# Kernel tuning notes

Hardware: AMD Instinct MI355X
Metric: run time of the kernel (lower is better)

## Reference

```python
import jax, jax.numpy as jnp
import numpy as np

EMB = 1280
MD = 200
N = 20000
E = 200000
LN_EPS = 1e-5


def _layer_norm(x, g, b):
    mu = jnp.mean(x, axis=-1, keepdims=True)
    var = jnp.mean((x - mu) ** 2, axis=-1, keepdims=True)
    return (x - mu) * jax.lax.rsqrt(var + LN_EPS) * g + b


def _gat_conv(x, edge_index, edge_attr, W, We, a_src, a_dst, a_edge, bias, heads, C):
    """PyG GATConv (bias-free lin, edge_dim, add_self_loops with fill='mean')."""
    n = x.shape[0]
    src, dst = edge_index[0], edge_index[1]
    # self-loop edge_attr = mean of incoming edge_attr per dst node (0 if none)
    cnt = jax.ops.segment_sum(jnp.ones((edge_attr.shape[0],), x.dtype), dst, n)
    s = jax.ops.segment_sum(edge_attr, dst, n)
    loop_attr = jnp.where(cnt[:, None] > 0, s / jnp.maximum(cnt, 1.0)[:, None], 0.0)
    loop = jnp.arange(n)
    src = jnp.concatenate([src, loop])
    dst = jnp.concatenate([dst, loop])
    ea = jnp.concatenate([edge_attr, loop_attr], axis=0)
    h = (x @ W).reshape(n, heads, C)                      # [N,H,C]
    al_s = jnp.einsum('nhc,hc->nh', h, a_src)
    al_d = jnp.einsum('nhc,hc->nh', h, a_dst)
    eh = (ea @ We).reshape(-1, heads, C)                  # [E+N,H,C]
    al_e = jnp.einsum('ehc,hc->eh', eh, a_edge)
    alpha = jax.nn.leaky_relu(al_s[src] + al_d[dst] + al_e, 0.2)
    amax = jax.ops.segment_max(alpha, dst, n)
    amax = jnp.where(jnp.isfinite(amax), amax, 0.0)
    ex = jnp.exp(alpha - amax[dst])
    denom = jax.ops.segment_sum(ex, dst, n)
    w = ex / (denom[dst] + 1e-16)                         # segment softmax over dst
    out = jax.ops.segment_sum(h[src] * w[:, :, None], dst, n)
    return out.reshape(n, heads * C) + bias


def _forward(x, edge_index, edge_attr,
             ca_qw, ca_qb, ca_kw, ca_kb, ca_vw, ca_vb, ca_ow, ca_ob,
             g0_w, g0_ew, g0_as, g0_ad, g0_ae, g0_b, ln0_g, ln0_b,
             g1_w, g1_ew, g1_as, g1_ad, g1_ae, g1_b, ln1_g, ln1_b,
             g2_w, g2_ew, g2_as, g2_ad, g2_ae, g2_b, ln2_g, ln2_b,
             cls_w1, cls_b1, cls_w2, cls_b2):
    xe = x[:, :EMB]
    md = x[0, EMB:]
    # CrossAttention: single md vector -> K,V are [1,hidden]
    Q = xe @ ca_qw + ca_qb                                # [N,hid]
    K = md @ ca_kw + ca_kb                                # [hid]
    V = md @ ca_vw + ca_vb                                # [hid]
    scores = (Q @ K) / jnp.sqrt(jnp.asarray(Q.shape[-1], Q.dtype))  # [N]
    wts = jax.nn.softmax(scores, axis=0)[:, None]         # softmax over nodes
    attended = wts * V[None, :]                           # [N,hid]
    h = attended @ ca_ow + ca_ob + xe                     # [N,EMB]

    h = _gat_conv(h, edge_index, edge_attr, g0_w, g0_ew, g0_as, g0_ad, g0_ae, g0_b, 4, 256)
    h = jax.nn.relu(_layer_norm(h, ln0_g, ln0_b))
    h = _gat_conv(h, edge_index, edge_attr, g1_w, g1_ew, g1_as, g1_ad, g1_ae, g1_b, 4, 256)
    h = jax.nn.relu(_layer_norm(h, ln1_g, ln1_b))
    h = _gat_conv(h, edge_index, edge_attr, g2_w, g2_ew, g2_as, g2_ad, g2_ae, g2_b, 1, 256)
    h = jax.nn.relu(_layer_norm(h, ln2_g, ln2_b))

    g = jnp.mean(h, axis=0, keepdims=True)                # [1,256]
    g = jax.nn.relu(g @ cls_w1 + cls_b1)
    return g @ cls_w2 + cls_b2                            # [1,2]


def setup_inputs() -> dict:
    key = jax.random.key(0)
    ks = jax.random.split(key, 64)
    i = [0]
    def nrm(shape, scale=0.05):
        i[0] += 1
        return jax.random.normal(ks[i[0]], shape, jnp.float32) * scale
    inp = {}
    inp['x'] = nrm((N, EMB + MD), 1.0)
    inp['edge_index'] = jax.random.randint(ks[60], (2, E), 0, N, jnp.int64 if jax.config.read('jax_enable_x64') else jnp.int32)
    inp['edge_attr'] = jax.random.uniform(ks[61], (E, 1), jnp.float32)
    inp.update(ca_qw=nrm((EMB, 256)), ca_qb=jnp.zeros((256,), jnp.float32),
               ca_kw=nrm((MD, 256)), ca_kb=jnp.zeros((256,), jnp.float32),
               ca_vw=nrm((MD, 256)), ca_vb=jnp.zeros((256,), jnp.float32),
               ca_ow=nrm((256, EMB)), ca_ob=jnp.zeros((EMB,), jnp.float32))
    inp.update(g0_w=nrm((EMB, 1024)), g0_ew=nrm((1, 1024)), g0_as=nrm((4, 256)),
               g0_ad=nrm((4, 256)), g0_ae=nrm((4, 256)), g0_b=jnp.zeros((1024,), jnp.float32),
               ln0_g=jnp.ones((1024,), jnp.float32), ln0_b=jnp.zeros((1024,), jnp.float32))
    inp.update(g1_w=nrm((1024, 1024)), g1_ew=nrm((1, 1024)), g1_as=nrm((4, 256)),
               g1_ad=nrm((4, 256)), g1_ae=nrm((4, 256)), g1_b=jnp.zeros((1024,), jnp.float32),
               ln1_g=jnp.ones((1024,), jnp.float32), ln1_b=jnp.zeros((1024,), jnp.float32))
    inp.update(g2_w=nrm((1024, 256)), g2_ew=nrm((1, 256)), g2_as=nrm((1, 256)),
               g2_ad=nrm((1, 256)), g2_ae=nrm((1, 256)), g2_b=jnp.zeros((256,), jnp.float32),
               ln2_g=jnp.ones((256,), jnp.float32), ln2_b=jnp.zeros((256,), jnp.float32))
    inp.update(cls_w1=nrm((256, 128)), cls_b1=jnp.zeros((128,), jnp.float32),
               cls_w2=nrm((128, 2)), cls_b2=jnp.zeros((2,), jnp.float32))
    return inp


def reference(x, edge_index, edge_attr,
              ca_qw, ca_qb, ca_kw, ca_kb, ca_vw, ca_vb, ca_ow, ca_ob,
              g0_w, g0_ew, g0_as, g0_ad, g0_ae, g0_b, ln0_g, ln0_b,
              g1_w, g1_ew, g1_as, g1_ad, g1_ae, g1_b, ln1_g, ln1_b,
              g2_w, g2_ew, g2_as, g2_ad, g2_ae, g2_b, ln2_g, ln2_b,
              cls_w1, cls_b1, cls_w2, cls_b2):
    return _forward(x, edge_index, edge_attr,
                    ca_qw, ca_qb, ca_kw, ca_kb, ca_vw, ca_vb, ca_ow, ca_ob,
                    g0_w, g0_ew, g0_as, g0_ad, g0_ae, g0_b, ln0_g, ln0_b,
                    g1_w, g1_ew, g1_as, g1_ad, g1_ae, g1_b, ln1_g, ln1_b,
                    g2_w, g2_ew, g2_as, g2_ad, g2_ae, g2_b, ln2_g, ln2_b,
                    cls_w1, cls_b1, cls_w2, cls_b2)
```

## Files before the change

### kernel.cpp

```cpp
#include <hip/hip_runtime.h>
#include <hip/hip_bf16.h>
#include <math.h>

#define N_NODES 20000
#define N_EDGES 200000
#define XROW    1480

typedef __attribute__((ext_vector_type(8))) _Float16 f16x8;
typedef __attribute__((ext_vector_type(8))) unsigned short u16x8;
typedef __attribute__((ext_vector_type(4))) float f32x4v;

__device__ __forceinline__ float wsum(float v){
#pragma unroll
  for (int o=32;o>0;o>>=1) v += __shfl_down(v,o);
  return v;
}
__device__ __forceinline__ float wmax(float v){
#pragma unroll
  for (int o=32;o>0;o>>=1) v = fmaxf(v,__shfl_down(v,o));
  return v;
}
__device__ __forceinline__ float wsum_all(float v){
#pragma unroll
  for (int o=32;o>0;o>>=1) v += __shfl_xor(v,o);
  return v;
}
__device__ __forceinline__ float wmax_all(float v){
#pragma unroll
  for (int o=32;o>0;o>>=1) v = fmaxf(v,__shfl_xor(v,o));
  return v;
}

__device__ __forceinline__ unsigned short f2hu(float f){
  _Float16 h = (_Float16)f;
  return __builtin_bit_cast(unsigned short, h);
}
__device__ __forceinline__ float hu2f(unsigned short u){
  return (float)__builtin_bit_cast(_Float16, u);
}

__device__ __forceinline__ void async_copy16(void* lds, const void* g){
  __builtin_amdgcn_global_load_lds((const __attribute__((address_space(1))) void*)g,
                                   (__attribute__((address_space(3))) void*)lds, 16, 0, 0);
}

__global__ void edge_count_kernel(const int* __restrict__ ei, const float* __restrict__ ea,
                                  int* __restrict__ cnt, float* __restrict__ easum, int E){
  int e = blockIdx.x*256 + threadIdx.x;
  if (e >= E) return;
  int dst = ei[E + e];
  atomicAdd(&cnt[dst], 1);
  atomicAdd(&easum[dst], ea[e]);
}

__launch_bounds__(1024)
__global__ void scan_kernel(const int* __restrict__ cnt, const float* __restrict__ easum,
                            int* __restrict__ off, float* __restrict__ loop_attr, int n){
  __shared__ int buf[1024];
  const int PER = (N_NODES + 1023)/1024;
  int t = threadIdx.x;
  int base = t*PER;
  int local[PER];
  int s = 0;
#pragma unroll
  for (int k=0;k<PER;k++){
    int i = base + k;
    int v = (i<n)? cnt[i] : 0;
    local[k] = v;
    s += v;
  }
  buf[t] = s;
  __syncthreads();
  for (int d2=1; d2<1024; d2<<=1){
    int tv = (t>=d2)? buf[t-d2] : 0;
    __syncthreads();
    buf[t] += tv;
    __syncthreads();
  }
  int run = buf[t] - s;
#pragma unroll
  for (int k=0;k<PER;k++){
    int i = base + k;
    if (i < n){
      off[i] = run;
      int v = local[k];
      loop_attr[i] = (v>0) ? easum[i]/(float)v : 0.f;
      run += v;
    }
  }
  if (t == 1023) off[n] = buf[1023];
}

__global__ void edge_fill_kernel(const int* __restrict__ ei, const float* __restrict__ ea,
                                 const int* __restrict__ off, int* __restrict__ fill,
                                 int* __restrict__ csr_src, float* __restrict__ csr_ea, int E){
  int e = blockIdx.x*256 + threadIdx.x;
  if (e >= E) return;
  int dst = ei[E + e];
  int pos = off[dst] + atomicAdd(&fill[dst], 1);
  csr_src[pos] = ei[e];
  csr_ea[pos]  = ea[e];
}

__global__ void wt_f16_kernel(const float* __restrict__ W, int K, int N,
                              unsigned short* __restrict__ Wt){
  __shared__ float tile[32][33];
  int k0 = blockIdx.x*32, n0 = blockIdx.y*32;
  int tx = threadIdx.x & 31, ty = threadIdx.x >> 5;
  for (int r=ty; r<32; r+=8) tile[r][tx] = W[(size_t)(k0+r)*N + n0+tx];
  __syncthreads();
  for (int r=ty; r<32; r+=8){
    float w = tile[tx][r];
    Wt[(size_t)(n0+r)*K + k0+tx] = f2hu(w);
  }
}

__global__ void kv_kernel(const float* __restrict__ x,
                          const float* __restrict__ kw, const float* __restrict__ kb,
                          const float* __restrict__ vw, const float* __restrict__ vb,
                          float* __restrict__ Kv, float* __restrict__ Vv){
  int j = threadIdx.x;
  float ka = kb[j], va = vb[j];
  for (int k=0;k<200;k++){
    float m = x[1280+k];
    ka = fmaf(m, kw[k*256+j], ka);
    va = fmaf(m, vw[k*256+j], va);
  }
  Kv[j]=ka; Vv[j]=va;
}

__global__ void qkvo_kernel(const float* __restrict__ qw, const float* __restrict__ ow,
                            const float* __restrict__ Kv, const float* __restrict__ Vv,
                            float* __restrict__ qK, float* __restrict__ Vo){
  int idx = blockIdx.x*256 + threadIdx.x;
  if (idx < 1280){
    float a=0;
    for (int j=0;j<256;j++) a = fmaf(qw[idx*256+j], Kv[j], a);
    qK[idx]=a;
  } else if (idx < 2560){
    int j = idx-1280;
    float a=0;
    for (int i=0;i<256;i++) a = fmaf(Vv[i], ow[(size_t)i*1280+j], a);
    Vo[j]=a;
  }
}

__global__ void obw_kernel(const float* __restrict__ ob, const float* __restrict__ Vo,
                           const float* __restrict__ W, float* __restrict__ obW, float* __restrict__ VoW){
  int j = blockIdx.x*256 + threadIdx.x;
  float a=0,b=0;
  for (int i=0;i<1280;i++){
    float w = W[(size_t)i*1024+j];
    a = fmaf(ob[i], w, a);
    b = fmaf(Vo[i], w, b);
  }
  obW[j]=a; VoW[j]=b;
}

__launch_bounds__(256)
__global__ void xh_scores_kernel(const float* __restrict__ x, const float* __restrict__ qK,
                                 unsigned short* __restrict__ xh, float* __restrict__ scores, int n){
  __shared__ float qs[1280];
  int t = threadIdx.x;
  for (int i=t;i<1280;i+=256) qs[i]=qK[i];
  __syncthreads();
  int wid = t>>6, lane = t&63;
  int node = blockIdx.x*4 + wid;
  if (node >= n) return;
  const float* xr = x + (size_t)node*XROW;
  unsigned short* orow = xh + (size_t)node*1280;
  float acc = 0.f;
#pragma unroll
  for (int it=0; it<5; it++){
    int c4 = it*64 + lane;
    float4 v = *(const float4*)(xr + c4*4);
    ushort4 o;
    o.x = f2hu(v.x); o.y = f2hu(v.y); o.z = f2hu(v.z); o.w = f2hu(v.w);
    *(ushort4*)(orow + c4*4) = o;
    acc = fmaf(v.x, qs[c4*4+0], acc);
    acc = fmaf(v.y, qs[c4*4+1], acc);
    acc = fmaf(v.z, qs[c4*4+2], acc);
    acc = fmaf(v.w, qs[c4*4+3], acc);
  }
  acc = wsum(acc);
  if (lane==0) scores[node] = acc;
}

__launch_bounds__(1024)
__global__ void softmax_nodes(const float* __restrict__ scores, float* __restrict__ wts, int n){
  __shared__ float red[16];
  int t = threadIdx.x, lane=t&63, wid=t>>6;
  float m = -INFINITY;
  for (int i=t;i<n;i+=1024) m = fmaxf(m, scores[i]);
  m = wmax(m);
  if (lane==0) red[wid]=m;
  __syncthreads();
  if (t==0){ float r=red[0]; for (int k=1;k<16;k++) r=fmaxf(r,red[k]); red[0]=r; }
  __syncthreads();
  float M = red[0];
  __syncthreads();
  float z=0;
  for (int i=t;i<n;i+=1024) z += __expf((scores[i]-M)*(1.f/16.f));
  z = wsum(z);
  if (lane==0) red[wid]=z;
  __syncthreads();
  if (t==0){ float r=0; for (int k=0;k<16;k++) r+=red[k]; red[0]=r; }
  __syncthreads();
  float invZ = 1.f/red[0];
  for (int i=t;i<n;i+=1024) wts[i] = __expf((scores[i]-M)*(1.f/16.f))*invZ;
}

__launch_bounds__(256)
__global__ void gemm_f16(const unsigned short* __restrict__ A,
                         const unsigned short* __restrict__ B,
                         unsigned short* __restrict__ C, int M, int N, int K,
                         const float* __restrict__ addCol,
                         const float* __restrict__ vCol,
                         const float* __restrict__ wRow,
                         const float* __restrict__ a_src,
                         const float* __restrict__ a_dst,
                         float* __restrict__ alsp,
                         float* __restrict__ aldp)
{
  __shared__ short lds[2*2*128*64];

  const int ntc = N >> 7;
  const int sh  = __popc(ntc - 1);
  const int g   = blockIdx.y >> sh;
  const int nt  = blockIdx.y & (ntc - 1);
  const int band = blockIdx.x + (g << 3);
  if (band * 128 >= M) return;

  const int t = threadIdx.x;
  const int w = t>>6, l = t&63;
  const int bm = band*128, bn = nt*128;
  const int wr = (w>>1)*64, wc = (w&1)*64;
  const int half = w & 1;

  f32x4v acc[4][4];
#pragma unroll
  for (int i=0;i<4;i++)
#pragma unroll
    for (int j=0;j<4;j++) acc[i][j] = (f32x4v){0.f,0.f,0.f,0.f};

  const unsigned short* Ap[4]; const unsigned short* Bp[4];
  int ldsOff[4];
#pragma unroll
  for (int q=0;q<4;q++){
    int p  = (w*4+q)*64 + l;
    int r  = p>>3, pc = p&7;
    int kc = (pc ^ (r&7))*8;
    int rowA = bm + r; if (rowA > M-1) rowA = M-1;
    Ap[q] = A + (size_t)rowA*K + kc;
    Bp[q] = B + (size_t)(bn+r)*K + kc;
    ldsOff[q] = (w*4+q)*64*8;
  }

  const int nsteps = K >> 6;

#pragma unroll
  for (int q=0;q<4;q++) async_copy16(lds + ldsOff[q],        Ap[q]);
#pragma unroll
  for (int q=0;q<4;q++) async_copy16(lds + 8192 + ldsOff[q], Bp[q]);

  const int q4 = l>>4, m16 = l&15;

  for (int ks0=0; ks0<nsteps; ++ks0){
    short* curb = lds + (ks0&1)*16384;

    if (ks0+1 < nsteps){
      short* nxt = lds + ((ks0+1)&1)*16384;
      const int k0n = (ks0+1)*64;
#pragma unroll
      for (int q=0;q<4;q++) async_copy16(nxt + ldsOff[q],        Ap[q] + k0n);
#pragma unroll
      for (int q=0;q<4;q++) async_copy16(nxt + 8192 + ldsOff[q], Bp[q] + k0n);
      asm volatile("s_waitcnt vmcnt(8)" ::: "memory");
    } else {
      asm volatile("s_waitcnt vmcnt(0)" ::: "memory");
    }
    __builtin_amdgcn_sched_barrier(0);
    __builtin_amdgcn_s_barrier();
    __builtin_amdgcn_sched_barrier(0);

    __builtin_amdgcn_s_setprio(1);
#pragma unroll
    for (int ks=0; ks<2; ks++){
      f16x8 af[4], bf[4];
      const int c = ks*4 + q4;
#pragma unroll
      for (int i=0;i<4;i++){
        int ra = wr + i*16 + m16;
        af[i] = *(const f16x8*)&curb[ra*64 + ((c ^ (ra&7))*8)];
        int rb = wc + i*16 + m16;
        bf[i] = *(const f16x8*)&curb[8192 + rb*64 + ((c ^ (rb&7))*8)];
      }
#pragma unroll
      for (int i=0;i<4;i++)
#pragma unroll
        for (int j=0;j<4;j++)
          acc[i][j] = __builtin_amdgcn_mfma_f32_16x16x32_f16(af[i], bf[j], acc[i][j], 0,0,0);
    }
    __builtin_amdgcn_s_setprio(0);
    __builtin_amdgcn_sched_barrier(0);
    __builtin_amdgcn_s_barrier();
    __builtin_amdgcn_sched_barrier(0);
  }

  float* sred = (float*)lds;
  float* dred = sred + 256;
  float asv[4], adv[4];
#pragma unroll
  for (int j=0;j<4;j++){
    int n = bn + wc + j*16 + m16;
    asv[j] = a_src[n];
    adv[j] = a_dst[n];
  }
#pragma unroll
  for (int i=0;i<4;i++){
#pragma unroll
    for (int r=0;r<4;r++){
      int rloc = wr + i*16 + q4*4 + r;
      int m = bm + rloc;
      float wrow = addCol ? wRow[m < M ? m : M-1] : 0.f;
      float vj[4];
#pragma unroll
      for (int j=0;j<4;j++){
        int n = bn + wc + j*16 + m16;
        float v = acc[i][j][r];
        if (addCol) v += addCol[n] + wrow*vCol[n];
        vj[j] = v;
      }
      if (m < M){
        unsigned short* crow = C + (size_t)m*N;
#pragma unroll
        for (int j=0;j<4;j++) crow[bn + wc + j*16 + m16] = f2hu(vj[j]);
      }
      float s = vj[0]*asv[0] + vj[1]*asv[1] + vj[2]*asv[2] + vj[3]*asv[3];
      float d = vj[0]*adv[0] + vj[1]*adv[1] + vj[2]*adv[2] + vj[3]*adv[3];
#pragma unroll
      for (int o=1;o<16;o<<=1){ s += __shfl_xor(s,o); d += __shfl_xor(d,o); }
      if (m16 == 0){
        sred[half*128 + rloc] = s;
        dred[half*128 + rloc] = d;
      }
    }
  }
  __syncthreads();
  if (t < 128){
    int m = bm + t;
    if (m < M){
      alsp[(size_t)nt*M + m] = sred[t] + sred[128+t];
      aldp[(size_t)nt*M + m] = dred[t] + dred[128+t];
    }
  }
}

__global__ void als_combine(const float* __restrict__ alsp, const float* __restrict__ aldp,
                            float* __restrict__ als, float* __restrict__ ald, int M, int H,
                            const float* __restrict__ We, const float* __restrict__ a_edge,
                            float* __restrict__ we){
  if (blockIdx.x == 0){
    int wid = threadIdx.x>>6, lane = threadIdx.x&63;
    if (wid < H){
      const float4* w4 = (const float4*)(We + wid*256);
      const float4* a4 = (const float4*)(a_edge + wid*256);
      float4 a = w4[lane], b = a4[lane];
      float v = a.x*b.x + a.y*b.y + a.z*b.z + a.w*b.w;
      v = wsum(v);
      if (lane==0) we[wid]=v;
    }
  }
  int idx = blockIdx.x*256 + threadIdx.x;
  if (idx >= M*H) return;
  int m = idx / H, hh = idx - m*H;
  als[idx] = alsp[(size_t)(2*hh)*M + m] + alsp[(size_t)(2*hh+1)*M + m];
  ald[idx] = aldp[(size_t)(2*hh)*M + m] + aldp[(size_t)(2*hh+1)*M + m];
}

template<int H>
__launch_bounds__(256)
__global__ void gat_agg_ln_wave(const unsigned short* __restrict__ hmat,
                           const float* __restrict__ als, const float* __restrict__ ald,
                           const int* __restrict__ off, const int* __restrict__ csr_src,
                           const float* __restrict__ csr_ea, const float* __restrict__ loop_attr,
                           const float* __restrict__ we,
                           const float* __restrict__ bias,
                           const float* __restrict__ ln_g, const float* __restrict__ ln_b,
                           float* __restrict__ outf, unsigned short* __restrict__ outb, int n)
{
  constexpr int OUT = 256*H;
  constexpr int CPL = OUT/64;
  const int wv = threadIdx.x>>6, lane = threadIdx.x&63;
  const int i = blockIdx.x*4 + wv;
  __shared__ float wbuf_s[4][64*H];
  __shared__ int   sbuf_s[4][64];
  if (i >= n) return;
  float* wbuf = wbuf_s[wv];
  int*   sbuf = sbuf_s[wv];

  const int begin = off[i];
  const int deg   = off[i+1]-begin;
  const int S     = deg + 1;

  float aldi[H], wei[H];
#pragma unroll
  for (int hh=0;hh<H;hh++){ aldi[hh]=ald[(size_t)i*H+hh]; wei[hh]=we[hh]; }
  const float lea = loop_attr[i];

  const int head = (lane*CPL) >> 8;
  const int c0   = lane*CPL;
  float acc[CPL];
#pragma unroll
  for (int c=0;c<CPL;c++) acc[c]=0.f;

  if (S <= 64){
    int src = i; float ev = lea;
    if (lane < deg){ src = csr_src[begin+lane]; ev = csr_ea[begin+lane]; }
    const bool act = lane < S;
    sbuf[lane] = src;

    if constexpr (CPL==16){
      u16x8 a0r0,a0r1,a1r0,a1r1;
      {
        const unsigned short* r0p = hmat + (size_t)sbuf[0]*OUT + c0;
        a0r0 = *(const u16x8*)r0p; a0r1 = *(const u16x8*)(r0p+8);
        a1r0 = a0r0; a1r1 = a0r1;
        if (S > 1){
          const unsigned short* r1p = hmat + (size_t)sbuf[1]*OUT + c0;
          a1r0 = *(const u16x8*)r1p; a1r1 = *(const u16x8*)(r1p+8);
        }
      }
      float a[H];
#pragma unroll
      for (int hh=0;hh<H;hh++){
        float v = als[(size_t)src*H+hh] + aldi[hh] + ev*wei[hh];
        a[hh] = v>0.f ? v : 0.2f*v;
      }
#pragma unroll
      for (int hh=0;hh<H;hh++){
        float M = wmax_all(act ? a[hh] : -INFINITY);
        float e = act ? __expf(a[hh]-M) : 0.f;
        float Z = wsum_all(e);
        wbuf[lane*H+hh] = e / (Z + 1e-16f);
      }
      int j = 0;
      for (; j+2<S; j+=2){
        u16x8 n0r0,n0r1,n1r0,n1r1;
        {
          const unsigned short* rp = hmat + (size_t)sbuf[j+2]*OUT + c0;
          n0r0 = *(const u16x8*)rp; n0r1 = *(const u16x8*)(rp+8);
          n1r0 = n0r0; n1r1 = n0r1;
          if (j+3 < S){
            const unsigned short* rq = hmat + (size_t)sbuf[j+3]*OUT + c0;
            n1r0 = *(const u16x8*)rq; n1r1 = *(const u16x8*)(rq+8);
          }
        }
        float w0 = wbuf[j*H+head], w1 = wbuf[(j+1)*H+head];
#pragma unroll
        for (int c=0;c<8;c++){
          acc[c]   = fmaf(w0, hu2f(a0r0[c]), acc[c]);
          acc[8+c] = fmaf(w0, hu2f(a0r1[c]), acc[8+c]);
        }
#pragma unroll
        for (int c=0;c<8;c++){
          acc[c]   = fmaf(w1, hu2f(a1r0[c]), acc[c]);
          acc[8+c] = fmaf(w1, hu2f(a1r1[c]), acc[8+c]);
        }
        a0r0=n0r0; a0r1=n0r1; a1r0=n1r0; a1r1=n1r1;
      }
      {
        float w0 = wbuf[j*H+head];
#pragma unroll
        for (int c=0;c<8;c++){
          acc[c]   = fmaf(w0, hu2f(a0r0[c]), acc[c]);
          acc[8+c] = fmaf(w0, hu2f(a0r1[c]), acc[8+c]);
        }
        if (j+1 < S){
          float w1 = wbuf[(j+1)*H+head];
#pragma unroll
          for (int c=0;c<8;c++){
            acc[c]   = fmaf(w1, hu2f(a1r0[c]), acc[c]);
            acc[8+c] = fmaf(w1, hu2f(a1r1[c]), acc[8+c]);
          }
        }
      }
    } else {
      ushort4 a0, a1;
      {
        a0 = *(const ushort4*)(hmat + (size_t)sbuf[0]*OUT + c0);
        a1 = a0;
        if (S > 1) a1 = *(const ushort4*)(hmat + (size_t)sbuf[1]*OUT + c0);
      }
      float a[H];
#pragma unroll
      for (int hh=0;hh<H;hh++){
        float v = als[(size_t)src*H+hh] + aldi[hh] + ev*wei[hh];
        a[hh] = v>0.f ? v : 0.2f*v;
      }
#pragma unroll
      for (int hh=0;hh<H;hh++){
        float M = wmax_all(act ? a[hh] : -INFINITY);
        float e = act ? __expf(a[hh]-M) : 0.f;
        float Z = wsum_all(e);
        wbuf[lane*H+hh] = e / (Z + 1e-16f);
      }
      int j = 0;
      for (; j+2<S; j+=2){
        ushort4 n0, n1;
        n0 = *(const ushort4*)(hmat + (size_t)sbuf[j+2]*OUT + c0);
        n1 = n0;
        if (j+3 < S) n1 = *(const ushort4*)(hmat + (size_t)sbuf[j+3]*OUT + c0);
        float w0 = wbuf[j*H+head], w1 = wbuf[(j+1)*H+head];
        acc[0]=fmaf(w0,hu2f(a0.x),acc[0]); acc[1]=fmaf(w0,hu2f(a0.y),acc[1]);
        acc[2]=fmaf(w0,hu2f(a0.z),acc[2]); acc[3]=fmaf(w0,hu2f(a0.w),acc[3]);
        acc[0]=fmaf(w1,hu2f(a1.x),acc[0]); acc[1]=fmaf(w1,hu2f(a1.y),acc[1]);
        acc[2]=fmaf(w1,hu2f(a1.z),acc[2]); acc[3]=fmaf(w1,hu2f(a1.w),acc[3]);
        a0=n0; a1=n1;
      }
      {
        float w0 = wbuf[j*H+head];
        acc[0]=fmaf(w0,hu2f(a0.x),acc[0]); acc[1]=fmaf(w0,hu2f(a0.y),acc[1]);
        acc[2]=fmaf(w0,hu2f(a0.z),acc[2]); acc[3]=fmaf(w0,hu2f(a0.w),acc[3]);
        if (j+1 < S){
          float w1 = wbuf[(j+1)*H+head];
          acc[0]=fmaf(w1,hu2f(a1.x),acc[0]); acc[1]=fmaf(w1,hu2f(a1.y),acc[1]);
          acc[2]=fmaf(w1,hu2f(a1.z),acc[2]); acc[3]=fmaf(w1,hu2f(a1.w),acc[3]);
        }
      }
    }
  } else {
    float rm[H];
#pragma unroll
    for (int hh=0;hh<H;hh++) rm[hh] = -INFINITY;
    for (int s=lane; s<S; s+=64){
      int src = (s<deg)? csr_src[begin+s] : i;
      float ev = (s<deg)? csr_ea[begin+s] : lea;
#pragma unroll
      for (int hh=0;hh<H;hh++){
        float v = als[(size_t)src*H+hh] + aldi[hh] + ev*wei[hh];
        v = v>0.f? v : 0.2f*v;
        rm[hh] = fmaxf(rm[hh], v);
      }
    }
    float M[H], es[H];
#pragma unroll
    for (int hh=0;hh<H;hh++){ M[hh]=wmax_all(rm[hh]); es[hh]=0.f; }
    for (int s=lane; s<S; s+=64){
      int src = (s<deg)? csr_src[begin+s] : i;
      float ev = (s<deg)? csr_ea[begin+s] : lea;
#pragma unroll
      for (int hh=0;hh<H;hh++){
        float v = als[(size_t)src*H+hh] + aldi[hh] + ev*wei[hh];
        v = v>0.f? v : 0.2f*v;
        es[hh] += __expf(v - M[hh]);
      }
    }
    float invZ[H];
#pragma unroll
    for (int hh=0;hh<H;hh++) invZ[hh] = 1.f/(wsum_all(es[hh]) + 1e-16f);
    for (int cb=0; cb<S; cb+=64){
      int m = min(64, S-cb);
      int s = cb + lane;
      if (s < S){
        int src = (s<deg)? csr_src[begin+s] : i;
        float ev = (s<deg)? csr_ea[begin+s] : lea;
        sbuf[lane] = src;
#pragma unroll
        for (int hh=0;hh<H;hh++){
          float v = als[(size_t)src*H+hh] + aldi[hh] + ev*wei[hh];
          v = v>0.f? v : 0.2f*v;
          wbuf[lane*H+hh] = __expf(v - M[hh]) * invZ[hh];
        }
      }
      for (int j=0;j<m;j++){
        int sj = sbuf[j];
        float wj = wbuf[j*H+head];
        const unsigned short* row = hmat + (size_t)sj*OUT + c0;
        if constexpr (CPL==16){
          u16x8 r0 = *(const u16x8*)(row);
          u16x8 r1 = *(const u16x8*)(row+8);
#pragma unroll
          for (int c=0;c<8;c++){
            acc[c]   = fmaf(wj, hu2f(r0[c]), acc[c]);
            acc[8+c] = fmaf(wj, hu2f(r1[c]), acc[8+c]);
          }
        } else {
          ushort4 r = *(const ushort4*)(row);
          acc[0]=fmaf(wj,hu2f(r.x),acc[0]); acc[1]=fmaf(wj,hu2f(r.y),acc[1]);
          acc[2]=fmaf(wj,hu2f(r.z),acc[2]); acc[3]=fmaf(wj,hu2f(r.w),acc[3]);
        }
      }
    }
  }

  float vals[CPL];
  float ls=0.f;
#pragma unroll
  for (int c=0;c<CPL;c+=4){
    float4 b4 = *(const float4*)(bias + c0 + c);
    vals[c]=acc[c]+b4.x; vals[c+1]=acc[c+1]+b4.y; vals[c+2]=acc[c+2]+b4.z; vals[c+3]=acc[c+3]+b4.w;
    ls += vals[c]+vals[c+1]+vals[c+2]+vals[c+3];
  }
  float mu = wsum_all(ls) * (1.f/OUT);
  float lv=0.f;
#pragma unroll
  for (int c=0;c<CPL;c++){ float d=vals[c]-mu; lv += d*d; }
  float inv = rsqrtf(wsum_all(lv)*(1.f/OUT) + 1e-5f);

  if (outb){
    if constexpr (CPL==16){
#pragma unroll
      for (int c=0;c<CPL;c+=8){
        u16x8 o;
#pragma unroll
        for (int k=0;k<8;k++){
          float g = ln_g[c0+c+k], b = ln_b[c0+c+k];
          o[k] = f2hu(fmaxf((vals[c+k]-mu)*inv*g + b, 0.f));
        }
        *(u16x8*)(outb + (size_t)i*OUT + c0 + c) = o;
      }
    } else {
      ushort4 o;
      o.x = f2hu(fmaxf((vals[0]-mu)*inv*ln_g[c0+0] + ln_b[c0+0], 0.f));
      o.y = f2hu(fmaxf((vals[1]-mu)*inv*ln_g[c0+1] + ln_b[c0+1], 0.f));
      o.z = f2hu(fmaxf((vals[2]-mu)*inv*ln_g[c0+2] + ln_b[c0+2], 0.f));
      o.w = f2hu(fmaxf((vals[3]-mu)*inv*ln_g[c0+3] + ln_b[c0+3], 0.f));
      *(ushort4*)(outb + (size_t)i*OUT + c0) = o;
    }
  } else {
#pragma unroll
    for (int c=0;c<CPL;c+=4){
      float4 g4 = *(const float4*)(ln_g + c0 + c);
      float4 b4 = *(const float4*)(ln_b + c0 + c);
      float4 o;
      o.x = fmaxf((vals[c+0]-mu)*inv*g4.x + b4.x, 0.f);
      o.y = fmaxf((vals[c+1]-mu)*inv*g4.y + b4.y, 0.f);
      o.z = fmaxf((vals[c+2]-mu)*inv*g4.z + b4.z, 0.f);
      o.w = fmaxf((vals[c+3]-mu)*inv*g4.w + b4.w, 0.f);
      *(float4*)(outf + (size_t)i*OUT + c0 + c) = o;
    }
  }
}

__global__ void colsum_kernel(const float* __restrict__ h2, float* __restrict__ gsum, int n){
  int c = threadIdx.x;
  float acc=0;
  for (int i=blockIdx.x;i<n;i+=gridDim.x) acc += h2[(size_t)i*256 + c];
  atomicAdd(&gsum[c], acc);
}

__launch_bounds__(128)
__global__ void cls_kernel(const float* __restrict__ gsum,
                           const float* __restrict__ w1, const float* __restrict__ b1,
                           const float* __restrict__ w2, const float* __restrict__ b2,
                           float* __restrict__ outp){
  __shared__ float g[256];
  __shared__ float hid[128];
  int t = threadIdx.x;
  g[t]     = gsum[t]    *(1.f/N_NODES);
  g[t+128] = gsum[t+128]*(1.f/N_NODES);
  __syncthreads();
  float a = b1[t];
  for (int c=0;c<256;c++) a = fmaf(g[c], w1[c*128+t], a);
  hid[t] = fmaxf(a, 0.f);
  __syncthreads();
  if (t<2){
    float o = b2[t];
    for (int j=0;j<128;j++) o = fmaf(hid[j], w2[j*2+t], o);
    outp[t] = o;
  }
}

extern "C" void kernel_launch(void* const* d_in, const int* in_sizes, int n_in,
                              void* d_out, int out_size, void* d_ws, size_t ws_size,
                              hipStream_t stream)
{
  const float* x      = (const float*)d_in[0];
  const int*   ei     = (const int*)  d_in[1];
  const float* ea     = (const float*)d_in[2];
  const float* ca_qw  = (const float*)d_in[3];
  const float* ca_kw  = (const float*)d_in[5];
  const float* ca_kb  = (const float*)d_in[6];
  const float* ca_vw  = (const float*)d_in[7];
  const float* ca_vb  = (const float*)d_in[8];
  const float* ca_ow  = (const float*)d_in[9];
  const float* ca_ob  = (const float*)d_in[10];
  const float* g0_w   = (const float*)d_in[11];
  const float* g0_ew  = (const float*)d_in[12];
  const float* g0_as  = (const float*)d_in[13];
  const float* g0_ad  = (const float*)d_in[14];
  const float* g0_ae  = (const float*)d_in[15];
  const float* g0_b   = (const float*)d_in[16];
  const float* ln0_g  = (const float*)d_in[17];
  const float* ln0_b  = (const float*)d_in[18];
  const float* g1_w   = (const float*)d_in[19];
  const float* g1_ew  = (const float*)d_in[20];
  const float* g1_as  = (const float*)d_in[21];
  const float* g1_ad  = (const float*)d_in[22];
  const float* g1_ae  = (const float*)d_in[23];
  const float* g1_b   = (const float*)d_in[24];
  const float* ln1_g  = (const float*)d_in[25];
  const float* ln1_b  = (const float*)d_in[26];
  const float* g2_w   = (const float*)d_in[27];
  const float* g2_ew  = (const float*)d_in[28];
  const float* g2_as  = (const float*)d_in[29];
  const float* g2_ad  = (const float*)d_in[30];
  const float* g2_ae  = (const float*)d_in[31];
  const float* g2_b   = (const float*)d_in[32];
  const float* ln2_g  = (const float*)d_in[33];
  const float* ln2_b  = (const float*)d_in[34];
  const float* cls_w1 = (const float*)d_in[35];
  const float* cls_b1 = (const float*)d_in[36];
  const float* cls_w2 = (const float*)d_in[37];
  const float* cls_b2 = (const float*)d_in[38];
  float* outp = (float*)d_out;

  const int N = N_NODES, E = N_EDGES;

  char* base = (char*)d_ws;
  size_t o = 0;
  auto alloc = [&](size_t bytes)->void*{
    void* p = base + o;
    o += (bytes + 255) & ~(size_t)255;
    return p;
  };
  unsigned short* hF   = (unsigned short*)alloc((size_t)N*1024*2);
  unsigned short* Af   = (unsigned short*)alloc((size_t)N*1280*2);
  float*          h2   = (float*)         alloc((size_t)N*256*4);
  unsigned short* Wt   = (unsigned short*)alloc((size_t)1280*1024*2);
  float* alsp      = (float*)alloc((size_t)8*N*4);
  float* aldp      = (float*)alloc((size_t)8*N*4);
  float* als       = (float*)alloc((size_t)2*N*4*4);
  float* ald       = als + (size_t)N*4;
  float* scores    = (float*)alloc((size_t)N*4);
  float* wts       = (float*)alloc((size_t)N*4);
  int*   cnt       = (int*)  alloc((size_t)N*4);
  float* easum     = (float*)alloc((size_t)N*4);
  int*   off       = (int*)  alloc((size_t)(N+1)*4);
  int*   fill      = (int*)  alloc((size_t)N*4);
  int*   csr_src   = (int*)  alloc((size_t)E*4);
  float* csr_ea    = (float*)alloc((size_t)E*4);
  float* loop_attr = (float*)alloc((size_t)N*4);
  float* Kv        = (float*)alloc(256*4);
  float* Vv        = (float*)alloc(256*4);
  float* qK        = (float*)alloc(1280*4);
  float* Vo        = (float*)alloc(1280*4);
  float* obW       = (float*)alloc(1024*4);
  float* VoW       = (float*)alloc(1024*4);
  float* web       = (float*)alloc(16*4);
  float* gsum      = (float*)alloc(256*4);

  hipMemsetAsync(cnt,   0, (size_t)N*4, stream);
  hipMemsetAsync(easum, 0, (size_t)N*4, stream);
  hipMemsetAsync(fill,  0, (size_t)N*4, stream);
  hipMemsetAsync(gsum,  0, 256*4,       stream);

  int eblocks = (E + 255)/256;
  edge_count_kernel<<<eblocks,256,0,stream>>>(ei, ea, cnt, easum, E);
  scan_kernel<<<1,1024,0,stream>>>(cnt, easum, off, loop_attr, N);
  edge_fill_kernel<<<eblocks,256,0,stream>>>(ei, ea, off, fill, csr_src, csr_ea, E);

  kv_kernel<<<1,256,0,stream>>>(x, ca_kw, ca_kb, ca_vw, ca_vb, Kv, Vv);
  qkvo_kernel<<<10,256,0,stream>>>(ca_qw, ca_ow, Kv, Vv, qK, Vo);
  xh_scores_kernel<<<(N+3)/4,256,0,stream>>>(x, qK, Af, scores, N);
  obw_kernel<<<4,256,0,stream>>>(ca_ob, Vo, g0_w, obW, VoW);
  softmax_nodes<<<1,1024,0,stream>>>(scores, wts, N);

  const int mTiles  = (N + 127)/128;
  const int mGroups = (mTiles + 7)/8;
  const int NB4 = (N + 3)/4;

  wt_f16_kernel<<<dim3(1280/32, 1024/32),256,0,stream>>>(g0_w, 1280, 1024, Wt);
  gemm_f16<<<dim3(8, mGroups*8),256,0,stream>>>(Af, Wt, hF, N, 1024, 1280, obW, VoW, wts,
                                                g0_as, g0_ad, alsp, aldp);
  als_combine<<<(N*4+255)/256,256,0,stream>>>(alsp, aldp, als, ald, N, 4, g0_ew, g0_ae, web);
  gat_agg_ln_wave<4><<<NB4,256,0,stream>>>(hF, als, ald, off, csr_src, csr_ea, loop_attr,
                                           web, g0_b, ln0_g, ln0_b, nullptr, Af, N);

  wt_f16_kernel<<<dim3(1024/32, 1024/32),256,0,stream>>>(g1_w, 1024, 1024, Wt);
  gemm_f16<<<dim3(8, mGroups*8),256,0,stream>>>(Af, Wt, hF, N, 1024, 1024, nullptr, nullptr, nullptr,
                                                g1_as, g1_ad, alsp, aldp);
  als_combine<<<(N*4+255)/256,256,0,stream>>>(alsp, aldp, als, ald, N, 4, g1_ew, g1_ae, web);
  gat_agg_ln_wave<4><<<NB4,256,0,stream>>>(hF, als, ald, off, csr_src, csr_ea, loop_attr,
                                           web, g1_b, ln1_g, ln1_b, nullptr, Af, N);

  wt_f16_kernel<<<dim3(1024/32, 256/32),256,0,stream>>>(g2_w, 1024, 256, Wt);
  gemm_f16<<<dim3(8, mGroups*2),256,0,stream>>>(Af, Wt, hF, N, 256, 1024, nullptr, nullptr, nullptr,
                                                g2_as, g2_ad, alsp, aldp);
  als_combine<<<(N+255)/256,256,0,stream>>>(alsp, aldp, als, ald, N, 1, g2_ew, g2_ae, web);
  gat_agg_ln_wave<1><<<NB4,256,0,stream>>>(hF, als, ald, off, csr_src, csr_ea, loop_attr,
                                           web, g2_b, ln2_g, ln2_b, h2, nullptr, N);

  colsum_kernel<<<256,256,0,stream>>>(h2, gsum, N);
  cls_kernel<<<1,128,0,stream>>>(gsum, cls_w1, cls_b1, cls_w2, cls_b2, outp);

  (void)in_sizes; (void)n_in; (void)out_size; (void)ws_size;
}
```

Before: 855.9 us.

## Add 256x256-tile GEMM with fused attention-logit reduction for GAT layers 0 and 1

Adds a new 512-thread GEMM kernel that uses 256x256 output tiles with double-buffered async LDS loads, an XOR-swizzled layout and phased MFMA issue. Its epilogue reduces the per-row source and destination attention logits across the four column-warps in LDS and writes them straight to als/ald. It also computes the edge-weight dot product, so the separate als_combine launch for the first two layers is no longer needed. Larger tiles raise operand reuse and cut global traffic, but the higher register pressure may lower occupancy, and with 8 column tiles' worth of fewer blocks there is a risk of wave-quantization imbalance.

```diff
diff --git a/kernel.cpp b/kernel.cpp
--- a/kernel.cpp
+++ b/kernel.cpp
@@ -208,6 +208,197 @@
   __syncthreads();
   float invZ = 1.f/red[0];
   for (int i=t;i<n;i+=1024) wts[i] = __expf((scores[i]-M)*(1.f/16.f))*invZ;
+}
+
+__launch_bounds__(512,2)
+__global__ void gemm256_f16(const unsigned short* __restrict__ A,
+                            const unsigned short* __restrict__ B,
+                            unsigned short* __restrict__ C, int M, int N, int K,
+                            const float* __restrict__ addCol,
+                            const float* __restrict__ vCol,
+                            const float* __restrict__ wRow,
+                            const float* __restrict__ a_src,
+                            const float* __restrict__ a_dst,
+                            float* __restrict__ als,
+                            float* __restrict__ ald,
+                            const float* __restrict__ We,
+                            const float* __restrict__ a_edge,
+                            float* __restrict__ we)
+{
+  __shared__ short lds[2*32768];
+
+  const int ntc = N >> 8;
+  const int sh  = (ntc==4)?2:((ntc==2)?1:0);
+  const int g   = blockIdx.y >> sh;
+  const int nt  = blockIdx.y & (ntc - 1);
+  const int band = blockIdx.x + (g << 3);
+  if (band * 256 >= M) return;
+
+  const int t = threadIdx.x;
+  const int w = t>>6, l = t&63;
+  const int bm = band*256, bn = nt*256;
+  const int wrh = w>>2;
+  const int wcl = (w&3)*64;
+  const int q4 = l>>4, m16 = l&15;
+
+  f32x4v acc[8][4];
+#pragma unroll
+  for (int i=0;i<8;i++)
+#pragma unroll
+    for (int j=0;j<4;j++) acc[i][j] = (f32x4v){0.f,0.f,0.f,0.f};
+
+  const unsigned short *pA00,*pA01,*pA10,*pA11,*pB00,*pB01,*pB10,*pB11;
+  int lA00,lA01,lA10,lA11,lB00,lB01,lB10,lB11;
+  {
+#pragma unroll
+    for (int half=0; half<2; half++){
+#pragma unroll
+      for (int q=0; q<2; q++){
+        int p  = (w*2+q)*64 + l;
+        int r  = p>>3, pc = p&7;
+        int kc = (pc ^ (r&7))*8;
+        int rowA = bm + half*128 + r; if (rowA > M-1) rowA = M-1;
+        int rowB = bn + half*128 + r;
+        const unsigned short* ap = A + (size_t)rowA*K + kc;
+        const unsigned short* bp = B + (size_t)rowB*K + kc;
+        int la = half*8192 + (w*2+q)*512;
+        int lb = 16384 + la;
+        if (half==0 && q==0){ pA00=ap; pB00=bp; lA00=la; lB00=lb; }
+        if (half==0 && q==1){ pA01=ap; pB01=bp; lA01=la; lB01=lb; }
+        if (half==1 && q==0){ pA10=ap; pB10=bp; lA10=la; lB10=lb; }
+        if (half==1 && q==1){ pA11=ap; pB11=bp; lA11=la; lB11=lb; }
+      }
+    }
+  }
+
+  const int nk = K >> 6;
+
+  {
+    short* b0 = lds;
+    async_copy16(b0 + lA00, pA00); async_copy16(b0 + lA01, pA01);
+    async_copy16(b0 + lA10, pA10); async_copy16(b0 + lA11, pA11);
+    async_copy16(b0 + lB00, pB00); async_copy16(b0 + lB01, pB01);
+    async_copy16(b0 + lB10, pB10); async_copy16(b0 + lB11, pB11);
+    asm volatile("s_waitcnt vmcnt(0)" ::: "memory");
+    __builtin_amdgcn_sched_barrier(0);
+    __builtin_amdgcn_s_barrier();
+    __builtin_amdgcn_sched_barrier(0);
+  }
+
+  for (int kt = 0; kt < nk; ++kt){
+    short* cur = lds + (kt&1)*32768;
+    short* nxt = lds + ((kt+1)&1)*32768;
+    const bool pre = (kt+1 < nk);
+    const size_t kofs = (size_t)(kt+1)*64;
+
+    f16x8 bf[4];
+#pragma unroll
+    for (int ph = 0; ph < 4; ++ph){
+      const int ks = ph >> 1, ih = ph & 1;
+      const int c  = ks*4 + q4;
+      f16x8 af[4];
+#pragma unroll
+      for (int ii=0; ii<4; ii++){
+        int rl = (ih*4+ii)*16 + m16;
+        af[ii] = *(const f16x8*)&cur[ wrh*8192 + rl*64 + ((c ^ (rl&7))*8) ];
+      }
+      if (ih == 0){
+#pragma unroll
+        for (int j=0;j<4;j++){
+          int rb = wcl + j*16 + m16;
+          bf[j] = *(const f16x8*)&cur[ 16384 + rb*64 + ((c ^ (rb&7))*8) ];
+        }
+      }
+      if (pre){
+        if (ph == 0){
+          async_copy16(nxt + lA00, pA00 + kofs); async_copy16(nxt + lA01, pA01 + kofs);
+          async_copy16(nxt + lA10, pA10 + kofs); async_copy16(nxt + lA11, pA11 + kofs);
+        } else if (ph == 1){
+          async_copy16(nxt + lB00, pB00 + kofs); async_copy16(nxt + lB01, pB01 + kofs);
+          async_copy16(nxt + lB10, pB10 + kofs); async_copy16(nxt + lB11, pB11 + kofs);
+        }
+      }
+      __builtin_amdgcn_sched_barrier(0);
+      __builtin_amdgcn_s_barrier();
+      asm volatile("s_waitcnt lgkmcnt(0)" ::: "memory");
+      __builtin_amdgcn_sched_barrier(0);
+
+      __builtin_amdgcn_s_setprio(1);
+#pragma unroll
+      for (int ii=0; ii<4; ii++)
+#pragma unroll
+        for (int j=0; j<4; j++)
+          acc[ih*4+ii][j] = __builtin_amdgcn_mfma_f32_16x16x32_f16(af[ii], bf[j], acc[ih*4+ii][j], 0,0,0);
+      __builtin_amdgcn_s_setprio(0);
+      __builtin_amdgcn_sched_barrier(0);
+      if (ph == 3){
+        asm volatile("s_waitcnt vmcnt(0)" ::: "memory");
+        __builtin_amdgcn_sched_barrier(0);
+      }
+      __builtin_amdgcn_s_barrier();
+      __builtin_amdgcn_sched_barrier(0);
+    }
+  }
+
+  __syncthreads();
+  float* sred = (float*)lds;
+  float* dred = sred + 1024;
+  const int bandc = w & 3;
+
+  float asv[4], adv[4];
+#pragma unroll
+  for (int j=0;j<4;j++){
+    int n = bn + wcl + j*16 + m16;
+    asv[j] = a_src[n];
+    adv[j] = a_dst[n];
+  }
+#pragma unroll
+  for (int i=0;i<8;i++){
+#pragma unroll
+    for (int r=0;r<4;r++){
+      int rloc = wrh*128 + i*16 + q4*4 + r;
+      int m = bm + rloc;
+      float wrow = addCol ? wRow[m < M ? m : M-1] : 0.f;
+      float vj[4];
+#pragma unroll
+      for (int j=0;j<4;j++){
+        int n = bn + wcl + j*16 + m16;
+        float v = acc[i][j][r];
+        if (addCol) v += addCol[n] + wrow*vCol[n];
+        vj[j] = v;
+      }
+      if (m < M){
+        unsigned short* crow = C + (size_t)m*N;
+#pragma unroll
+        for (int j=0;j<4;j++) crow[bn + wcl + j*16 + m16] = f2hu(vj[j]);
+      }
+      float s = vj[0]*asv[0] + vj[1]*asv[1] + vj[2]*asv[2] + vj[3]*asv[3];
+      float d = vj[0]*adv[0] + vj[1]*adv[1] + vj[2]*adv[2] + vj[3]*adv[3];
+#pragma unroll
+      for (int o=1;o<16;o<<=1){ s += __shfl_xor(s,o); d += __shfl_xor(d,o); }
+      if (m16 == 0){
+        sred[bandc*256 + rloc] = s;
+        dred[bandc*256 + rloc] = d;
+      }
+    }
+  }
+  __syncthreads();
+  if (t < 256){
+    int m = bm + t;
+    if (m < M){
+      float s = sred[t] + sred[256+t] + sred[512+t] + sred[768+t];
+      float d = dred[t] + dred[256+t] + dred[512+t] + dred[768+t];
+      als[(size_t)m*ntc + nt] = s;
+      ald[(size_t)m*ntc + nt] = d;
+    }
+  }
+  if (band == 0 && nt == 0 && w < ntc){
+    float4 a = ((const float4*)(We + w*256))[l];
+    float4 b = ((const float4*)(a_edge + w*256))[l];
+    float v = a.x*b.x + a.y*b.y + a.z*b.z + a.w*b.w;
+    v = wsum(v);
+    if (l==0) we[w]=v;
+  }
 }
 
 __launch_bounds__(256)
@@ -769,19 +960,19 @@
 
   const int mTiles  = (N + 127)/128;
   const int mGroups = (mTiles + 7)/8;
+  const int mT256   = (N + 255)/256;
+  const int mG256   = (mT256 + 7)/8;
   const int NB4 = (N + 3)/4;
 
   wt_f16_kernel<<<dim3(1280/32, 1024/32),256,0,stream>>>(g0_w, 1280, 1024, Wt);
-  gemm_f16<<<dim3(8, mGroups*8),256,0,stream>>>(Af, Wt, hF, N, 1024, 1280, obW, VoW, wts,
-                                                g0_as, g0_ad, alsp, aldp);
-  als_combine<<<(N*4+255)/256,256,0,stream>>>(alsp, aldp, als, ald, N, 4, g0_ew, g0_ae, web);
+  gemm256_f16<<<dim3(8, mG256*4),512,0,stream>>>(Af, Wt, hF, N, 1024, 1280, obW, VoW, wts,
+                                                 g0_as, g0_ad, als, ald, g0_ew, g0_ae, web);
   gat_agg_ln_wave<4><<<NB4,256,0,stream>>>(hF, als, ald, off, csr_src, csr_ea, loop_attr,
                                            web, g0_b, ln0_g, ln0_b, nullptr, Af, N);
 
   wt_f16_kernel<<<dim3(1024/32, 1024/32),256,0,stream>>>(g1_w, 1024, 1024, Wt);
-  gemm_f16<<<dim3(8, mGroups*8),256,0,stream>>>(Af, Wt, hF, N, 1024, 1024, nullptr, nullptr, nullptr,
-                                                g1_as, g1_ad, alsp, aldp);
-  als_combine<<<(N*4+255)/256,256,0,stream>>>(alsp, aldp, als, ald, N, 4, g1_ew, g1_ae, web);
+  gemm256_f16<<<dim3(8, mG256*4),512,0,stream>>>(Af, Wt, hF, N, 1024, 1024, nullptr, nullptr, nullptr,
+                                                 g1_as, g1_ad, als, ald, g1_ew, g1_ae, web);
   gat_agg_ln_wave<4><<<NB4,256,0,stream>>>(hF, als, ald, off, csr_src, csr_ea, loop_attr,
                                            web, g1_b, ln1_g, ln1_b, nullptr, Af, N);
 
```

Result: slower. 901.2 us (+5.3%).
